# Kernel optimization log

Measured on AMD Instinct MI355X. Metric: run time of the kernel, lower is better.

The kernel has to match this reference:

```python
import jax, jax.numpy as jnp
import numpy as np

B, T, D, H, L, E, NL = 512, 360, 12, 256, 64, 8, 2


def _lstm_layer(x, h0, c0, Wih, Whh, bih, bhh):
    # x: [B, T, in_dim]; PyTorch gate order i, f, g, o
    b = bih + bhh
    def step(carry, xt):
        h, c = carry
        gates = xt @ Wih.T + h @ Whh.T + b  # [B, 4H]
        i, f, g, o = jnp.split(gates, 4, axis=-1)
        c = jax.nn.sigmoid(f) * c + jax.nn.sigmoid(i) * jnp.tanh(g)
        h = jax.nn.sigmoid(o) * jnp.tanh(c)
        return (h, c), h
    (hT, cT), ys = jax.lax.scan(step, (h0, c0), jnp.swapaxes(x, 0, 1))
    return jnp.swapaxes(ys, 0, 1), hT, cT


def _forward(x, eps, emb, Wih0f, Whh0f, bih0f, bhh0f, Wih0b, Whh0b, bih0b, bhh0b,
             Wih1f, Whh1f, bih1f, bhh1f, Wih1b, Whh1b, bih1b, bhh1b,
             Wmu, bmu, Wlv, blv, Whid, bhid, Wcell, bcell,
             dWih0, dWhh0, dbih0, dbhh0, dWih1, dWhh1, dbih1, dbhh1, Wout, bout, labels):
    Bn = x.shape[0]
    ce = emb[labels]  # [B, E]
    xc = jnp.concatenate([x, jnp.broadcast_to(ce[:, None, :], (Bn, T, E))], axis=-1)
    z0 = jnp.zeros((Bn, H), x.dtype)
    # encoder: 2-layer bidirectional LSTM
    yf0, _, _ = _lstm_layer(xc, z0, z0, Wih0f, Whh0f, bih0f, bhh0f)
    yb0, _, _ = _lstm_layer(xc[:, ::-1], z0, z0, Wih0b, Whh0b, bih0b, bhh0b)
    y0 = jnp.concatenate([yf0, yb0[:, ::-1]], axis=-1)  # [B, T, 2H]
    _, hf, _ = _lstm_layer(y0, z0, z0, Wih1f, Whh1f, bih1f, bhh1f)
    _, hb, _ = _lstm_layer(y0[:, ::-1], z0, z0, Wih1b, Whh1b, bih1b, bhh1b)
    hcat = jnp.concatenate([hf, hb], axis=-1)  # [B, 2H]
    mu = hcat @ Wmu.T + bmu
    logvar = hcat @ Wlv.T + blv
    z = mu + eps * jnp.exp(0.5 * logvar)
    zc = jnp.concatenate([z, ce], axis=-1)  # [B, L+E]
    # faithful to torch .view(num_layers, B, H) on a [B, NL*H] tensor (row-major reshape)
    hid = (zc @ Whid.T + bhid).reshape(NL, Bn, H)
    cel = (zc @ Wcell.T + bcell).reshape(NL, Bn, H)
    # decoder with full teacher forcing: step-t input is target step t-1 (zeros at t=0)
    shifted = jnp.concatenate([jnp.zeros((Bn, 1, D), x.dtype), x[:, :-1]], axis=1)
    din = jnp.concatenate([shifted, jnp.broadcast_to(zc[:, None, :], (Bn, T, L + E))], axis=-1)
    y0d, _, _ = _lstm_layer(din, hid[0], cel[0], dWih0, dWhh0, dbih0, dbhh0)
    y1d, _, _ = _lstm_layer(y0d, hid[1], cel[1], dWih1, dWhh1, dbih1, dbhh1)
    x_recon = y1d @ Wout.T + bout
    return x_recon, mu, logvar, z


def setup_inputs():
    key = jax.random.key(0)
    ki = iter(jax.random.split(key, 48))
    def rn(shape, s=0.05):
        return jax.random.normal(next(ki), shape, jnp.float32) * s
    inp = {}
    inp["x"] = jax.random.normal(next(ki), (B, T, D), jnp.float32)
    inp["labels"] = jax.random.randint(next(ki), (B,), 0, 2)
    inp["eps"] = jax.random.normal(next(ki), (B, L), jnp.float32)
    inp["emb"] = rn((2, E), 1.0)
    # encoder LSTM: layer0 input D+E, layer1 input 2H, forward/backward directions
    for name, idim in [("0f", D + E), ("0b", D + E), ("1f", 2 * H), ("1b", 2 * H)]:
        inp["Wih" + name] = rn((4 * H, idim))
        inp["Whh" + name] = rn((4 * H, H))
        inp["bih" + name] = rn((4 * H,))
        inp["bhh" + name] = rn((4 * H,))
    inp["Wmu"] = rn((L, 2 * H)); inp["bmu"] = rn((L,))
    inp["Wlv"] = rn((L, 2 * H)); inp["blv"] = rn((L,))
    inp["Whid"] = rn((NL * H, L + E)); inp["bhid"] = rn((NL * H,))
    inp["Wcell"] = rn((NL * H, L + E)); inp["bcell"] = rn((NL * H,))
    # decoder LSTM: layer0 input D + (L+E), layer1 input H
    inp["dWih0"] = rn((4 * H, D + L + E)); inp["dWhh0"] = rn((4 * H, H))
    inp["dbih0"] = rn((4 * H,)); inp["dbhh0"] = rn((4 * H,))
    inp["dWih1"] = rn((4 * H, H)); inp["dWhh1"] = rn((4 * H, H))
    inp["dbih1"] = rn((4 * H,)); inp["dbhh1"] = rn((4 * H,))
    inp["Wout"] = rn((D, H)); inp["bout"] = rn((D,))
    return inp


def reference(x, labels, eps, emb, Wih0f, Whh0f, bih0f, bhh0f, Wih0b, Whh0b, bih0b, bhh0b,
              Wih1f, Whh1f, bih1f, bhh1f, Wih1b, Whh1b, bih1b, bhh1b,
              Wmu, bmu, Wlv, blv, Whid, bhid, Wcell, bcell,
              dWih0, dWhh0, dbih0, dbhh0, dWih1, dWhh1, dbih1, dbhh1, Wout, bout):
    return _forward(x, eps, emb, Wih0f, Whh0f, bih0f, bhh0f, Wih0b, Whh0b, bih0b, bhh0b,
                    Wih1f, Whh1f, bih1f, bhh1f, Wih1b, Whh1b, bih1b, bhh1b,
                    Wmu, bmu, Wlv, blv, Whid, bhid, Wcell, bcell,
                    dWih0, dWhh0, dbih0, dbhh0, dWih1, dWhh1, dbih1, dbhh1, Wout, bout, labels)
```

## Files before the change

kernel.cpp:

```cpp
#include <hip/hip_runtime.h>
#include <cstdint>
#include <cstddef>

#define TT 360
#define BFULL 512
#define GH 1024

typedef unsigned short u16;
typedef short bf16x8_t __attribute__((ext_vector_type(8)));
typedef short bf16x4_t __attribute__((ext_vector_type(4)));
typedef float f32x4_t  __attribute__((ext_vector_type(4)));

#define MFMA(A,B,C) __builtin_amdgcn_mfma_f32_16x16x32_bf16(A,B,C,0,0,0)

__device__ __forceinline__ float bf2f(u16 u){
  union { unsigned u; float f; } v; v.u = ((unsigned)u) << 16; return v.f;
}
__device__ __forceinline__ u16 f2bf(float f){
  union { float f; unsigned u; } v; v.f = f;
  unsigned r = v.u + 0x7FFFu + ((v.u >> 16) & 1u);
  return (u16)(r >> 16);
}
__device__ __forceinline__ float sigm(float x){
  float e = __builtin_amdgcn_exp2f(-1.44269504089f * x);
  return __builtin_amdgcn_rcpf(1.f + e);
}
__device__ __forceinline__ float tanh_(float x){
  float e = __builtin_amdgcn_exp2f(-2.88539008178f * x);
  return 2.f * __builtin_amdgcn_rcpf(1.f + e) - 1.f;
}
__device__ __forceinline__ f32x4_t cvt4(bf16x4_t v){
  f32x4_t r;
#pragma unroll
  for (int i = 0; i < 4; ++i) r[i] = bf2f((u16)v[i]);
  return r;
}

__device__ __forceinline__ void st_u16_sc(void* p, u16 v){
  asm volatile("global_store_short %0, %1, off sc0 sc1" :: "v"(p), "v"(v) : "memory");
}
__device__ __forceinline__ void st_flag(int* p, int v){
  asm volatile("global_store_dword %0, %1, off sc0 sc1" :: "v"(p), "v"(v) : "memory");
}
__device__ __forceinline__ int ld_flag(const int* p){
  int v;
  asm volatile("global_load_dword %0, %1, off sc0 sc1\n\ts_waitcnt vmcnt(0)"
               : "=v"(v) : "v"(p) : "memory");
  return v;
}
__device__ __forceinline__ void ld2_b128_sc(const void* p0, const void* p1, f32x4_t* a, f32x4_t* b){
  asm volatile("global_load_dwordx4 %0, %2, off sc0 sc1\n\t"
               "global_load_dwordx4 %1, %3, off sc0 sc1\n\t"
               "s_waitcnt vmcnt(0)"
               : "=&v"(*a), "=&v"(*b) : "v"(p0), "v"(p1) : "memory");
}


__global__ void k_cvt_pad(const float* src, u16* dst, int N, int srcK, int useK, int Np, int Kp){
  int i = blockIdx.x * blockDim.x + threadIdx.x;
  if (i >= Np * Kp) return;
  int n = i / Kp, k = i - n * Kp;
  float v = (n < N && k < useK) ? src[(size_t)n * srcK + k] : 0.f;
  dst[i] = f2bf(v);
}

__global__ void k_repack(const float* src, u16* dst){
  int d = blockIdx.x * blockDim.x + threadIdx.x;
  if (d >= 262144) return;
  int e  = d & 7;
  int ln = (d >> 3) & 63;
  int ks = (d >> 9) & 7;
  int ct = (d >> 12) & 3;
  int g  = (d >> 14) & 3;
  int ns = (d >> 16) & 3;
  int c = ns * 64 + ct * 16 + (ln & 15);
  int n = g * 256 + c;
  int k = ks * 32 + (ln >> 4) * 8 + e;
  dst[d] = f2bf(src[n * 256 + k]);
}

__global__ void k_bias_sum(const float* a, const float* b, float* o, int n){
  int i = blockIdx.x * blockDim.x + threadIdx.x;
  if (i < n) o[i] = a[i] + b[i];
}

__global__ void k_zero(int* p, int n){
  int i = blockIdx.x * blockDim.x + threadIdx.x;
  if (i < n) p[i] = 0;
}


struct ProjArgs {
  const u16* A; const u16* W;
  const float* colbias;
  u16* G;
  int Akp, K, t0, rev, Bg, bgLog;
};

template<int BK>
__global__ __launch_bounds__(256) void k_proj(ProjArgs p){
  constexpr int SLOTS = BK / 8;
  constexpr int SM = SLOTS - 1;
  constexpr int LOG = (BK == 64) ? 3 : 2;
  __shared__ __align__(16) u16 lA[128 * BK];
  __shared__ __align__(16) u16 lW[128 * BK];
  const int tid = threadIdx.x, lane = tid & 63, wid = tid >> 6;
  const int wm = wid >> 1, wn = wid & 1;
  const int mBase = blockIdx.x * 128;
  const int nBase = blockIdx.y * 128;
  const int t_rel = mBase >> p.bgLog;
  const int bBase = mBase & (p.Bg - 1);
  const int t_glob = p.t0 + t_rel;
  const int t_src = p.rev ? (TT - 1 - t_glob) : t_glob;

  f32x4_t acc[4][4];
#pragma unroll
  for (int m = 0; m < 4; ++m)
#pragma unroll
    for (int n = 0; n < 4; ++n) acc[m][n] = (f32x4_t){0.f, 0.f, 0.f, 0.f};

  for (int k0 = 0; k0 < p.K; k0 += BK){
#pragma unroll
    for (int i = 0; i < (128 * SLOTS) / 256; ++i){
      int idx = i * 256 + tid;
      int row = idx >> LOG, sl = idx & SM;
      bf16x8_t va = *(const bf16x8_t*)(p.A + (size_t)((bBase + row) * TT + t_src) * p.Akp + k0 + sl * 8);
      *(bf16x8_t*)&lA[((row << LOG) + (sl ^ (row & SM))) * 8] = va;
      bf16x8_t vw = *(const bf16x8_t*)(p.W + (size_t)(nBase + row) * p.K + k0 + sl * 8);
      *(bf16x8_t*)&lW[((row << LOG) + (sl ^ (row & SM))) * 8] = vw;
    }
    __syncthreads();
#pragma unroll
    for (int kk = 0; kk < BK; kk += 32){
      bf16x8_t af[4], wf[4];
#pragma unroll
      for (int m = 0; m < 4; ++m){
        int row = wm * 64 + m * 16 + (lane & 15);
        int sl = ((kk >> 3) + (lane >> 4)) ^ (row & SM);
        af[m] = *(const bf16x8_t*)&lA[((row << LOG) + sl) * 8];
      }
#pragma unroll
      for (int n = 0; n < 4; ++n){
        int row = wn * 64 + n * 16 + (lane & 15);
        int sl = ((kk >> 3) + (lane >> 4)) ^ (row & SM);
        wf[n] = *(const bf16x8_t*)&lW[((row << LOG) + sl) * 8];
      }
#pragma unroll
      for (int m = 0; m < 4; ++m)
#pragma unroll
        for (int n = 0; n < 4; ++n)
          acc[m][n] = MFMA(af[m], wf[n], acc[m][n]);
    }
    __syncthreads();
  }

  const int btiles = p.Bg >> 4;
#pragma unroll
  for (int m = 0; m < 4; ++m){
    int btile = (bBase + wm * 64 + m * 16) >> 4;
#pragma unroll
    for (int n = 0; n < 4; ++n){
      int coltile = nBase + wn * 64 + n * 16;
      int col = coltile + (lane & 15);
      int ntile = coltile >> 4;
      float cb = p.colbias ? p.colbias[col] : 0.f;
      bf16x4_t outv;
#pragma unroll
      for (int q = 0; q < 4; ++q)
        outv[q] = (short)f2bf(acc[m][n][q] + cb);
      *(bf16x4_t*)(p.G + ((((size_t)t_rel * btiles + btile) * 64 + ntile) * 64 + lane) * 4) = outv;
    }
  }
}


struct RecArgs {
  const u16* Wr0; const u16* Wr1;
  int* flg0; int* flg1;
  u16* hX0; u16* hX1;
  const u16* G0; const u16* G1; int btilesG;
  const float* x; const int* labels; const float* emb; int gb0;
  const float* cb0; const float* cb1;
  const u16* Wx0; const u16* Wx1;
  const u16* zcF;
  const u16* hI0; const u16* hI1;
  const float* cI0; const float* cI1;
  float* cS0; float* cS1;
  u16* hW0; u16* hW1;
  u16* Y; int ycols; int yoff0; int yoff1;
  const u16* Wo; const float* bo; float* outp;
  int t0, t1, nbt;
};

template<int MODE>
__global__ __launch_bounds__(512, 1) void k_rec(RecArgs a){
  constexpr bool XIN  = (MODE <= 1);
  constexpr bool DEC  = (MODE == 1);
  constexpr bool GIN  = (MODE >= 2);
  constexpr bool OUTP = (MODE == 3);

  __shared__ __align__(16) u16 Wlds[65536];
  __shared__ __align__(16) u16 hlds[8192];
  __shared__ __align__(16) u16 xT[1024];

  const int bx = blockIdx.x;
  const int ns = bx & 3;
  const int gid = bx >> 2;
  const int dir = gid / a.nbt;
  const int bt = gid - dir * a.nbt;
  const int bb = bt * 32;
  const int tid = threadIdx.x;
  const int lane = tid & 63, w = tid >> 6;
  const int l15 = lane & 15, lhi = lane >> 4;
  const int mt = w >> 2, ct = w & 3;
  const int colb = ns * 64 + ct * 16 + l15;

  const u16* Wsrc = (dir ? a.Wr1 : a.Wr0) + (size_t)ns * 65536;
  int* flg = (dir ? a.flg1 : a.flg0) + bt * 4;
  u16* hXg = (dir ? a.hX1 : a.hX0) + (size_t)bt * 16384;
  const int yoff = dir ? a.yoff1 : a.yoff0;

#pragma unroll
  for (int i = 0; i < 16; ++i){
    int idx = i * 512 + tid;
    *(f32x4_t*)((char*)Wlds + (size_t)idx * 16) = *(const f32x4_t*)((const char*)Wsrc + (size_t)idx * 16);
  }

  float cfr[4];
  {
    const float* cp = dir ? a.cI1 : a.cI0;
#pragma unroll
    for (int q = 0; q < 4; ++q)
      cfr[q] = cp ? cp[(size_t)(bb + mt * 16 + lhi * 4 + q) * 256 + colb] : 0.f;
  }

  float bias4[4];
  f32x4_t zcv[4];
  bf16x8_t wfx[4];
  if (XIN && !DEC){
    const float* cb = dir ? a.cb1 : a.cb0;
#pragma unroll
    for (int g = 0; g < 4; ++g) bias4[g] = cb[g * 256 + colb];
  }
  if (DEC){
#pragma unroll
    for (int g = 0; g < 4; ++g){
      int ntile = g * 16 + ns * 4 + ct;
      bf16x4_t zv = *(const bf16x4_t*)(a.zcF + ((((size_t)((bb >> 4) + mt)) * 64 + ntile) * 64 + lane) * 4);
      zcv[g] = cvt4(zv);
    }
  }
  if (XIN){
    const u16* Wx = dir ? a.Wx1 : a.Wx0;
#pragma unroll
    for (int g = 0; g < 4; ++g)
      wfx[g] = *(const bf16x8_t*)(Wx + (size_t)(g * 256 + colb) * 32 + lhi * 8);
  }
  bf16x8_t wo8[8];
  float bo = 0.f;
  if (OUTP && ns == 0 && w < 2){
#pragma unroll
    for (int ks = 0; ks < 8; ++ks)
      wo8[ks] = *(const bf16x8_t*)(a.Wo + (size_t)l15 * 256 + ks * 32 + lhi * 8);
    if (l15 < 12) bo = a.bo[l15];
  }

  if (XIN){
    int row = tid >> 4, c16 = tid & 15;
    int gr = a.gb0 + bb + row;
    u16 vA = 0, vB = 0;
    if (!DEC){
      int lb = a.labels[gr];
      if (c16 >= 12) vA = f2bf(a.emb[lb * 8 + (c16 - 12)]);
      if (c16 < 4)   vB = f2bf(a.emb[lb * 8 + 4 + c16]);
    }
    u16 x0 = 0;
    if (!DEC && c16 < 12){
      int t0src = dir ? (TT - 1) : 0;
      x0 = f2bf(a.x[((size_t)gr * TT + t0src) * 12 + c16]);
    }
    xT[row * 32 + c16] = (c16 < 12) ? x0 : vA;
    xT[row * 32 + 16 + c16] = vB;
  }

  unsigned dsA[8];
#pragma unroll
  for (int ks = 0; ks < 8; ++ks)
    dsA[ks] = (unsigned)((((mt * 16 + l15) << 5) + (((ks << 2) + lhi) ^ (l15 & 7))) * 16);
  unsigned wrO[4];
#pragma unroll
  for (int q = 0; q < 4; ++q){
    int row = mt * 16 + lhi * 4 + q;
    wrO[q] = (unsigned)((row << 9) + (((colb >> 3) ^ (row & 7)) << 4) + ((colb & 7) << 1));
  }
  const char* Gc = GIN ? (const char*)(dir ? a.G1 : a.G0) : nullptr;
  unsigned gOff[4];
  const unsigned gstep = (unsigned)a.btilesG * 32768u;
  bf16x4_t gvP[4];
  if (GIN){
#pragma unroll
    for (int g = 0; g < 4; ++g){
      int ntile = g * 16 + ns * 4 + ct;
      gOff[g] = (unsigned)((((bb >> 4) + mt) * 64 + ntile) * 512 + lane * 8);
    }
#pragma unroll
    for (int g = 0; g < 4; ++g)
      gvP[g] = *(const bf16x4_t*)(Gc + gOff[g]);
  }

  if (a.t0 == 0){
    const u16* hp = dir ? a.hI1 : a.hI0;
#pragma unroll
    for (int q = 0; q < 4; ++q){
      u16 hv = hp ? hp[(size_t)(bb + mt * 16 + lhi * 4 + q) * 256 + colb] : (u16)0;
      st_u16_sc((char*)hXg + wrO[q], hv);
    }
  }
  __syncthreads();
  if (tid == 0 && a.t0 == 0) st_flag(flg + ns, 1);

  auto spin_to = [&](int target){
    if (w == 0){
      while (true){
        int f = (lane < 4) ? ld_flag(flg + lane) : target;
        if (__all(f >= target)) break;
        __builtin_amdgcn_s_sleep(2);
      }
    }
    __syncthreads();
  };
  auto stage_h = [&](int par){
    const char* src = (const char*)hXg + par * 16384;
    int o0 = (w * 2) * 1024 + lane * 16;
    f32x4_t v0, v1;
    ld2_b128_sc(src + o0, src + o0 + 1024, &v0, &v1);
    *(f32x4_t*)((char*)hlds + o0) = v0;
    *(f32x4_t*)((char*)hlds + o0 + 1024) = v1;
  };

  spin_to(a.t0 + 1);
  stage_h(a.t0 & 1);
  __syncthreads();

  for (int t = a.t0; t < a.t1; ++t){
    if (OUTP && ns == 0 && w < 2 && t > 0){
      f32x4_t oa = (f32x4_t){0.f, 0.f, 0.f, 0.f};
#pragma unroll
      for (int ks = 0; ks < 8; ++ks){
        bf16x8_t af = *(const bf16x8_t*)((char*)hlds + w * 8192 + dsA[ks]);
        oa = MFMA(af, wo8[ks], oa);
      }
      if (l15 < 12){
#pragma unroll
        for (int q = 0; q < 4; ++q)
          a.outp[((size_t)(bb + w * 16 + lhi * 4 + q) * TT + (t - 1)) * 12 + l15] = oa[q] + bo;
      }
    }
    f32x4_t acc[4];
    if (GIN){
#pragma unroll
      for (int g = 0; g < 4; ++g) acc[g] = cvt4(gvP[g]);
    } else if (DEC){
#pragma unroll
      for (int g = 0; g < 4; ++g) acc[g] = zcv[g];
    } else {
#pragma unroll
      for (int g = 0; g < 4; ++g) acc[g] = (f32x4_t){bias4[g], bias4[g], bias4[g], bias4[g]};
    }
    if (XIN){
      bf16x8_t ax = *(const bf16x8_t*)((char*)xT + (mt * 16 + l15) * 64 + lhi * 16);
#pragma unroll
      for (int g = 0; g < 4; ++g) acc[g] = MFMA(ax, wfx[g], acc[g]);
    }
#pragma unroll
    for (int ks = 0; ks < 8; ++ks){
      bf16x8_t af = *(const bf16x8_t*)((char*)hlds + dsA[ks]);
#pragma unroll
      for (int g = 0; g < 4; ++g){
        bf16x8_t bf = *(const bf16x8_t*)((char*)Wlds + ((g * 4 + ct) * 8 + ks) * 1024 + lane * 16);
        acc[g] = MFMA(af, bf, acc[g]);
      }
    }
    const int par = (t + 1) & 1;
    u16 hbv[4];
#pragma unroll
    for (int q = 0; q < 4; ++q){
      float iv = sigm(acc[0][q]);
      float fv = sigm(acc[1][q]);
      float gv = tanh_(acc[2][q]);
      float ov = sigm(acc[3][q]);
      float c = fv * cfr[q] + iv * gv;
      cfr[q] = c;
      u16 hb = f2bf(ov * tanh_(c));
      hbv[q] = hb;
      st_u16_sc((char*)hXg + par * 16384 + wrO[q], hb);
    }
    __syncthreads();
    if (tid == 0) st_flag(flg + ns, t + 2);
    if (XIN){
      const int ty = (MODE == 0 && dir) ? (TT - 1 - t) : t;
#pragma unroll
      for (int q = 0; q < 4; ++q)
        a.Y[((size_t)(bb + mt * 16 + lhi * 4 + q) * TT + ty) * a.ycols + yoff + colb] = hbv[q];
    }
    if (GIN){
#pragma unroll
      for (int g = 0; g < 4; ++g) gOff[g] += gstep;
      if (t + 1 < a.t1){
#pragma unroll
        for (int g = 0; g < 4; ++g)
          gvP[g] = *(const bf16x4_t*)(Gc + gOff[g]);
      }
    }
    spin_to(t + 2);
    stage_h(par);
    if (XIN && (t + 1) < a.t1){
      if (tid < 128 && (tid & 3) < 3){
        int row = tid >> 2, xq = tid & 3;
        int tsrc = DEC ? t : (dir ? (TT - 2 - t) : (t + 1));
        f32x4_t xv = *(const f32x4_t*)(a.x + ((size_t)(a.gb0 + bb + row) * TT + tsrc) * 12 + xq * 4);
        bf16x4_t xb;
#pragma unroll
        for (int e = 0; e < 4; ++e) xb[e] = (short)f2bf(xv[e]);
        *(bf16x4_t*)((char*)xT + row * 64 + xq * 8) = xb;
      }
    }
    __syncthreads();
  }

  if (OUTP && ns == 0 && w < 2){
    f32x4_t oa = (f32x4_t){0.f, 0.f, 0.f, 0.f};
#pragma unroll
    for (int ks = 0; ks < 8; ++ks){
      bf16x8_t af = *(const bf16x8_t*)((char*)hlds + w * 8192 + dsA[ks]);
      oa = MFMA(af, wo8[ks], oa);
    }
    if (l15 < 12){
#pragma unroll
      for (int q = 0; q < 4; ++q)
        a.outp[((size_t)(bb + w * 16 + lhi * 4 + q) * TT + (a.t1 - 1)) * 12 + l15] = oa[q] + bo;
    }
  }
  {
    float* cs = dir ? a.cS1 : a.cS0;
    if (cs){
#pragma unroll
      for (int q = 0; q < 4; ++q)
        cs[(size_t)(bb + mt * 16 + lhi * 4 + q) * 256 + colb] = cfr[q];
    }
    u16* hw = dir ? a.hW1 : a.hW0;
    if (hw){
#pragma unroll
      for (int q = 0; q < 4; ++q){
        u16 hv = *(u16*)((char*)hlds + wrO[q]);
        hw[(size_t)(bb + mt * 16 + lhi * 4 + q) * 256 + colb] = hv;
      }
    }
  }
}


__global__ void k_mulv(const u16* sH0, const u16* sH1,
                       const float* Wmu, const float* bmu,
                       const float* Wlv, const float* blv, float* mulv){
  int i = blockIdx.x * blockDim.x + threadIdx.x;
  if (i >= BFULL * 128) return;
  int b = i >> 7, j = i & 127;
  const float* W = (j < 64) ? (Wmu + (size_t)j * 512) : (Wlv + (size_t)(j - 64) * 512);
  float s = (j < 64) ? bmu[j] : blv[j - 64];
  for (int k = 0; k < 256; ++k) s += bf2f(sH0[(size_t)b * 256 + k]) * W[k];
  for (int k = 0; k < 256; ++k) s += bf2f(sH1[(size_t)b * 256 + k]) * W[256 + k];
  mulv[i] = s;
}

__global__ void k_sample(const float* mulv, const float* eps, const int* labels, const float* emb,
                         float* out_mu, float* out_lv, float* out_z, float* zcf){
  int i = blockIdx.x * blockDim.x + threadIdx.x;
  if (i >= BFULL * 128) return;
  int b = i >> 7, j = i & 127;
  if (j < 64){
    float mu = mulv[b * 128 + j];
    float lv = mulv[b * 128 + 64 + j];
    float z = mu + eps[b * 64 + j] * __expf(0.5f * lv);
    out_mu[b * 64 + j] = mu;
    out_lv[b * 64 + j] = lv;
    out_z[b * 64 + j] = z;
    zcf[i] = z;
  } else if (j < 72){
    zcf[i] = emb[labels[b] * 8 + (j - 64)];
  } else {
    zcf[i] = 0.f;
  }
}

__global__ void k_hc(const float* zcf, const float* Whid, const float* bhid,
                     const float* Wcell, const float* bcell, float* HC){
  int i = blockIdx.x * blockDim.x + threadIdx.x;
  if (i >= BFULL * 1024) return;
  int b = i >> 10, n = i & 1023;
  const float* W; float s;
  if (n < 512){ W = Whid + (size_t)n * 72; s = bhid[n]; }
  else        { W = Wcell + (size_t)(n - 512) * 72; s = bcell[n - 512]; }
  for (int k = 0; k < 72; ++k) s += zcf[b * 128 + k] * W[k];
  HC[i] = s;
}

__global__ void k_zconst(const float* zcf, const float* dWih0,
                         const float* dbih0, const float* dbhh0, float* zconst){
  int i = blockIdx.x * blockDim.x + threadIdx.x;
  if (i >= BFULL * 1024) return;
  int b = i >> 10, n = i & 1023;
  float s = dbih0[n] + dbhh0[n];
  const float* W = dWih0 + (size_t)n * 84 + 12;
  for (int k = 0; k < 72; ++k) s += zcf[b * 128 + k] * W[k];
  zconst[i] = s;
}

__global__ void k_zfrag(const float* zconst, u16* zcF){
  int i = blockIdx.x * blockDim.x + threadIdx.x;
  if (i >= BFULL * GH) return;
  int q = i & 3, ln = (i >> 2) & 63, nt = (i >> 8) & 63, bt = i >> 14;
  int r = bt * 16 + (ln >> 4) * 4 + q;
  int col = nt * 16 + (ln & 15);
  zcF[i] = f2bf(zconst[(size_t)r * GH + col]);
}

__global__ void k_dec_init(const float* HC, u16* h0, float* c0, u16* h1, float* c1){
  int i = blockIdx.x * blockDim.x + threadIdx.x;
  if (i >= BFULL * 256) return;
  int b = i >> 8, h = i & 255;
  int col = (b & 1) * 256 + h;
  int r0 = b >> 1;
  int r1 = 256 + (b >> 1);
  h0[i] = f2bf(HC[(size_t)r0 * 1024 + col]);
  c0[i] =      HC[(size_t)r0 * 1024 + 512 + col];
  h1[i] = f2bf(HC[(size_t)r1 * 1024 + col]);
  c1[i] =      HC[(size_t)r1 * 1024 + 512 + col];
}


static inline size_t alignup(size_t x){ return (x + 255) & ~(size_t)255; }
static inline int ilog2(int x){ return 31 - __builtin_clz((unsigned)x); }

extern "C" void kernel_launch(void* const* d_in, const int* in_sizes, int n_in,
                              void* d_out, int out_size, void* d_ws, size_t ws_size,
                              hipStream_t stream){
  const float* x      = (const float*)d_in[0];
  const int*   labels = (const int*)  d_in[1];
  const float* eps    = (const float*)d_in[2];
  const float* emb    = (const float*)d_in[3];
  const float* Wih0f = (const float*)d_in[4],  *Whh0f = (const float*)d_in[5];
  const float* bih0f = (const float*)d_in[6],  *bhh0f = (const float*)d_in[7];
  const float* Wih0b = (const float*)d_in[8],  *Whh0b = (const float*)d_in[9];
  const float* bih0b = (const float*)d_in[10], *bhh0b = (const float*)d_in[11];
  const float* Wih1f = (const float*)d_in[12], *Whh1f = (const float*)d_in[13];
  const float* bih1f = (const float*)d_in[14], *bhh1f = (const float*)d_in[15];
  const float* Wih1b = (const float*)d_in[16], *Whh1b = (const float*)d_in[17];
  const float* bih1b = (const float*)d_in[18], *bhh1b = (const float*)d_in[19];
  const float* Wmu = (const float*)d_in[20], *bmu = (const float*)d_in[21];
  const float* Wlv = (const float*)d_in[22], *blv = (const float*)d_in[23];
  const float* Whid = (const float*)d_in[24], *bhid = (const float*)d_in[25];
  const float* Wcell = (const float*)d_in[26], *bcell = (const float*)d_in[27];
  const float* dWih0 = (const float*)d_in[28], *dWhh0 = (const float*)d_in[29];
  const float* dbih0 = (const float*)d_in[30], *dbhh0 = (const float*)d_in[31];
  const float* dWih1 = (const float*)d_in[32], *dWhh1 = (const float*)d_in[33];
  const float* dbih1 = (const float*)d_in[34], *dbhh1 = (const float*)d_in[35];
  const float* Wout = (const float*)d_in[36], *bout = (const float*)d_in[37];

  float* out = (float*)d_out;
  float* out_mu = out + (size_t)BFULL * TT * 12;
  float* out_lv = out_mu + (size_t)BFULL * 64;
  float* out_z  = out_lv + (size_t)BFULL * 64;

  char* ws = (char*)d_ws; size_t off = 0;
  auto alloc = [&](size_t bytes)->char*{ char* p = ws + off; off += alignup(bytes); return p; };

  u16* W0f_b  = (u16*)alloc(1024 * 32 * 2);
  u16* W0b_b  = (u16*)alloc(1024 * 32 * 2);
  u16* dWx_b  = (u16*)alloc(1024 * 32 * 2);
  u16* Wo_b   = (u16*)alloc(16 * 256 * 2);
  u16* Whh0f_r = (u16*)alloc((size_t)1024 * 256 * 2);
  u16* Whh0b_r = (u16*)alloc((size_t)1024 * 256 * 2);
  u16* Whh1f_r = (u16*)alloc((size_t)1024 * 256 * 2);
  u16* Whh1b_r = (u16*)alloc((size_t)1024 * 256 * 2);
  u16* dWhh0_r = (u16*)alloc((size_t)1024 * 256 * 2);
  u16* dWhh1_r = (u16*)alloc((size_t)1024 * 256 * 2);
  u16* dWih1_b = (u16*)alloc((size_t)1024 * 256 * 2);
  u16* Wih1f_b = (u16*)alloc((size_t)1024 * 512 * 2);
  u16* Wih1b_b = (u16*)alloc((size_t)1024 * 512 * 2);
  float* b0f = (float*)alloc(1024 * 4);
  float* b0b = (float*)alloc(1024 * 4);
  float* b1f = (float*)alloc(1024 * 4);
  float* b1b = (float*)alloc(1024 * 4);
  float* db1 = (float*)alloc(1024 * 4);
  u16*  sHe1 = (u16*)alloc((size_t)2 * BFULL * 256 * 2);
  float* sCe1 = (float*)alloc((size_t)2 * BFULL * 256 * 4);
  u16*  dh0 = (u16*)alloc((size_t)BFULL * 256 * 2);
  float* dc0 = (float*)alloc((size_t)BFULL * 256 * 4);
  u16*  dh1 = (u16*)alloc((size_t)BFULL * 256 * 2);
  float* dc1 = (float*)alloc((size_t)BFULL * 256 * 4);
  float* mulv = (float*)alloc((size_t)BFULL * 128 * 4);
  float* zcf  = (float*)alloc((size_t)BFULL * 128 * 4);
  float* HC   = (float*)alloc((size_t)BFULL * 1024 * 4);
  float* zconst = (float*)alloc((size_t)BFULL * 1024 * 4);
  u16*  zcF   = (u16*)alloc((size_t)BFULL * 1024 * 2);
  int*  flagsA = (int*)alloc(512 * 4);
  u16*  hXA    = (u16*)alloc((size_t)2 * 16 * 16384 * 2);

  size_t rem = (ws_size > off + (1 << 20)) ? ws_size - off - (1 << 20) : 0;
  int eb = 128, Tc = 2;
  {
    const int sch[][2] = {
      {512,360},{512,120},{512,40},{512,24},{512,12},{512,8},
      {256,360},{256,120},{256,40},{256,12},{256,8},
      {128,360},{128,40},{128,8},{128,2}};
    for (int i = 0; i < (int)(sizeof(sch)/sizeof(sch[0])); ++i){
      size_t need = alignup((size_t)sch[i][0] * TT * 512 * 2)
                  + 2 * alignup((size_t)sch[i][1] * sch[i][0] * GH * 2);
      if (need <= rem){ eb = sch[i][0]; Tc = sch[i][1]; break; }
    }
  }
  const int ebLog = ilog2(eb);
  const int nGroups = BFULL / eb;
  const int nbt = eb / 32;

  u16* y0 = (u16*)alloc((size_t)eb * TT * 512 * 2);
  u16* Gf = (u16*)alloc((size_t)Tc * eb * GH * 2);
  u16* Gb = (u16*)alloc((size_t)Tc * eb * GH * 2);
  u16* y0d = y0;

  auto cvt = [&](const float* src, u16* dst, int N, int srcK, int useK, int Np, int Kp){
    int tot = Np * Kp;
    k_cvt_pad<<<(tot + 255) / 256, 256, 0, stream>>>(src, dst, N, srcK, useK, Np, Kp);
  };
  auto repack = [&](const float* src, u16* dst){
    k_repack<<<1024, 256, 0, stream>>>(src, dst);
  };
  auto bsum = [&](const float* a, const float* b, float* o){
    k_bias_sum<<<4, 256, 0, stream>>>(a, b, o, 1024);
  };
  auto proj = [&](const u16* A, int Akp, int K, const u16* W, const float* cbp,
                  u16* G, int t0, int tc, int rev){
    ProjArgs pa; pa.A = A; pa.W = W; pa.colbias = cbp; pa.G = G;
    pa.Akp = Akp; pa.K = K; pa.t0 = t0; pa.rev = rev; pa.Bg = eb; pa.bgLog = ebLog;
    dim3 grid(tc * (eb / 128), 8);
    k_proj<64><<<grid, 256, 0, stream>>>(pa);
  };
  auto flgbase = [&](int layer, int d, int gb0){ return flagsA + ((layer * 2 + d) * 16 + (gb0 >> 5)) * 4; };
  auto hxbase  = [&](int d, int gb0){ return hXA + ((size_t)d * 16 + (gb0 >> 5)) * 16384; };

  k_zero<<<2, 256, 0, stream>>>(flagsA, 512);
  cvt(Wih0f, W0f_b, 1024, 20, 20, 1024, 32);
  cvt(Wih0b, W0b_b, 1024, 20, 20, 1024, 32);
  cvt(dWih0, dWx_b, 1024, 84, 12, 1024, 32);
  cvt(Wout,  Wo_b,  12, 256, 256, 16, 256);
  repack(Whh0f, Whh0f_r);
  repack(Whh0b, Whh0b_r);
  repack(Whh1f, Whh1f_r);
  repack(Whh1b, Whh1b_r);
  repack(dWhh0, dWhh0_r);
  repack(dWhh1, dWhh1_r);
  cvt(dWih1, dWih1_b, 1024, 256, 256, 1024, 256);
  cvt(Wih1f, Wih1f_b, 1024, 512, 512, 1024, 512);
  cvt(Wih1b, Wih1b_b, 1024, 512, 512, 1024, 512);
  bsum(bih0f, bhh0f, b0f);
  bsum(bih0b, bhh0b, b0b);
  bsum(bih1f, bhh1f, b1f);
  bsum(bih1b, bhh1b, b1b);
  bsum(dbih1, dbhh1, db1);

  for (int g = 0; g < nGroups; ++g){
    int gb0 = g * eb;
    {
      RecArgs ra = {};
      ra.Wr0 = Whh0f_r; ra.Wr1 = Whh0b_r;
      ra.flg0 = flgbase(0, 0, gb0); ra.flg1 = flgbase(0, 1, gb0);
      ra.hX0 = hxbase(0, gb0); ra.hX1 = hxbase(1, gb0);
      ra.x = x; ra.labels = labels; ra.emb = emb; ra.gb0 = gb0;
      ra.cb0 = b0f; ra.cb1 = b0b;
      ra.Wx0 = W0f_b; ra.Wx1 = W0b_b;
      ra.Y = y0; ra.ycols = 512; ra.yoff0 = 0; ra.yoff1 = 256;
      ra.t0 = 0; ra.t1 = TT; ra.nbt = nbt;
      k_rec<0><<<2 * nbt * 4, 512, 0, stream>>>(ra);
    }
    for (int t0 = 0; t0 < TT; t0 += Tc){
      int t1 = (t0 + Tc < TT) ? t0 + Tc : TT; int tc = t1 - t0;
      proj(y0, 512, 512, Wih1f_b, b1f, Gf, t0, tc, 0);
      proj(y0, 512, 512, Wih1b_b, b1b, Gb, t0, tc, 1);
      RecArgs ra = {};
      ra.Wr0 = Whh1f_r; ra.Wr1 = Whh1b_r;
      ra.flg0 = flgbase(1, 0, gb0); ra.flg1 = flgbase(1, 1, gb0);
      ra.hX0 = hxbase(0, gb0); ra.hX1 = hxbase(1, gb0);
      ra.G0 = Gf; ra.G1 = Gb; ra.btilesG = eb >> 4;
      ra.cI0 = t0 ? (sCe1 + (size_t)gb0 * 256) : nullptr;
      ra.cI1 = t0 ? (sCe1 + (size_t)BFULL * 256 + (size_t)gb0 * 256) : nullptr;
      ra.cS0 = sCe1 + (size_t)gb0 * 256;
      ra.cS1 = sCe1 + (size_t)BFULL * 256 + (size_t)gb0 * 256;
      ra.hW0 = sHe1 + (size_t)gb0 * 256;
      ra.hW1 = sHe1 + (size_t)BFULL * 256 + (size_t)gb0 * 256;
      ra.t0 = t0; ra.t1 = t1; ra.nbt = nbt;
      k_rec<2><<<2 * nbt * 4, 512, 0, stream>>>(ra);
    }
  }

  k_mulv<<<(BFULL * 128) / 256, 256, 0, stream>>>(sHe1, sHe1 + (size_t)BFULL * 256,
                                                  Wmu, bmu, Wlv, blv, mulv);
  k_sample<<<(BFULL * 128) / 256, 256, 0, stream>>>(mulv, eps, labels, emb,
                                                    out_mu, out_lv, out_z, zcf);
  k_hc<<<(BFULL * 1024) / 256, 256, 0, stream>>>(zcf, Whid, bhid, Wcell, bcell, HC);
  k_zconst<<<(BFULL * 1024) / 256, 256, 0, stream>>>(zcf, dWih0, dbih0, dbhh0, zconst);
  k_zfrag<<<(BFULL * GH) / 256, 256, 0, stream>>>(zconst, zcF);
  k_dec_init<<<(BFULL * 256) / 256, 256, 0, stream>>>(HC, dh0, dc0, dh1, dc1);

  for (int g = 0; g < nGroups; ++g){
    int gb0 = g * eb;
    {
      RecArgs ra = {};
      ra.Wr0 = dWhh0_r; ra.Wr1 = dWhh0_r;
      ra.flg0 = flgbase(2, 0, gb0); ra.flg1 = flgbase(2, 0, gb0);
      ra.hX0 = hxbase(0, gb0); ra.hX1 = hxbase(0, gb0);
      ra.x = x; ra.gb0 = gb0;
      ra.zcF = zcF + ((size_t)(gb0 >> 4)) * 16384;
      ra.Wx0 = dWx_b; ra.Wx1 = dWx_b;
      ra.hI0 = dh0 + (size_t)gb0 * 256;
      ra.cI0 = dc0 + (size_t)gb0 * 256;
      ra.Y = y0d; ra.ycols = 256; ra.yoff0 = 0; ra.yoff1 = 0;
      ra.t0 = 0; ra.t1 = TT; ra.nbt = nbt;
      k_rec<1><<<nbt * 4, 512, 0, stream>>>(ra);
    }
    for (int t0 = 0; t0 < TT; t0 += Tc){
      int t1 = (t0 + Tc < TT) ? t0 + Tc : TT; int tc = t1 - t0;
      proj(y0d, 256, 256, dWih1_b, db1, Gf, t0, tc, 0);
      RecArgs ra = {};
      ra.Wr0 = dWhh1_r; ra.Wr1 = dWhh1_r;
      ra.flg0 = flgbase(3, 0, gb0); ra.flg1 = flgbase(3, 0, gb0);
      ra.hX0 = hxbase(0, gb0); ra.hX1 = hxbase(0, gb0);
      ra.G0 = Gf; ra.G1 = Gf; ra.btilesG = eb >> 4;
      ra.hI0 = dh1 + (size_t)gb0 * 256;
      ra.cI0 = t0 ? (sCe1 + (size_t)gb0 * 256) : (dc1 + (size_t)gb0 * 256);
      ra.cS0 = sCe1 + (size_t)gb0 * 256;
      ra.Wo = Wo_b; ra.bo = bout;
      ra.outp = out + (size_t)gb0 * TT * 12;
      ra.t0 = t0; ra.t1 = t1; ra.nbt = nbt;
      k_rec<3><<<nbt * 4, 512, 0, stream>>>(ra);
    }
  }
}
```

Baseline: 5.783 ms.

## Fuse decoder layer-1 recurrence into layer-0 kernel as wavefront-pipelined blocks

Decoder layer 0 and layer 1 now run concurrently in a single persistent launch. Extra blocks compute layer 1 one step behind layer 0, synchronised through global flags. Layer 1's input and recurrent weights are concatenated into one K=512 LDS-resident matrix, so the separate chunked input-projection GEMM and its G buffer are dropped. The output head now lives in the layer-1 blocks. The cost is 1.5x more co-resident blocks, extra cross-layer flag spinning, and higher per-block MFMA work for layer 1, with a deadlock risk if not all blocks are co-resident.

Result: faster. 4.934 ms, median of 2 (-14.7%).

```diff
diff --git a/kernel.cpp b/kernel.cpp
--- a/kernel.cpp
+++ b/kernel.cpp
@@ -53,6 +53,16 @@
                "global_load_dwordx4 %1, %3, off sc0 sc1\n\t"
                "s_waitcnt vmcnt(0)"
                : "=&v"(*a), "=&v"(*b) : "v"(p0), "v"(p1) : "memory");
+}
+__device__ __forceinline__ void ld4_b128_sc(const void* p0, const void* p1, const void* p2, const void* p3,
+                                            f32x4_t* a, f32x4_t* b, f32x4_t* c, f32x4_t* d){
+  asm volatile("global_load_dwordx4 %0, %4, off sc0 sc1\n\t"
+               "global_load_dwordx4 %1, %5, off sc0 sc1\n\t"
+               "global_load_dwordx4 %2, %6, off sc0 sc1\n\t"
+               "global_load_dwordx4 %3, %7, off sc0 sc1\n\t"
+               "s_waitcnt vmcnt(0)"
+               : "=&v"(*a), "=&v"(*b), "=&v"(*c), "=&v"(*d)
+               : "v"(p0), "v"(p1), "v"(p2), "v"(p3) : "memory");
 }
 
 
@@ -77,6 +87,21 @@
   int n = g * 256 + c;
   int k = ks * 32 + (ln >> 4) * 8 + e;
   dst[d] = f2bf(src[n * 256 + k]);
+}
+
+__global__ void k_repack_cat(const float* Wih, const float* Whh, u16* dst){
+  int d = blockIdx.x * blockDim.x + threadIdx.x;
+  if (d >= 524288) return;
+  int e   = d & 7;
+  int ln  = (d >> 3) & 63;
+  int ks  = (d >> 9) & 15;
+  int ct  = (d >> 13) & 1;
+  int g   = (d >> 14) & 3;
+  int ns8 = (d >> 16) & 7;
+  int n = g * 256 + ns8 * 32 + ct * 16 + (ln & 15);
+  int k = ks * 32 + (ln >> 4) * 8 + e;
+  float v = (k < 256) ? Wih[(size_t)n * 256 + k] : Whh[(size_t)n * 256 + (k - 256)];
+  dst[d] = f2bf(v);
 }
 
 __global__ void k_bias_sum(const float* a, const float* b, float* o, int n){
@@ -194,36 +219,190 @@
 
 template<int MODE>
 __global__ __launch_bounds__(512, 1) void k_rec(RecArgs a){
+  constexpr bool ENC0 = (MODE == 0);
+  constexpr bool DEC  = (MODE == 1);
+  constexpr bool GIN  = (MODE == 2);
   constexpr bool XIN  = (MODE <= 1);
-  constexpr bool DEC  = (MODE == 1);
-  constexpr bool GIN  = (MODE >= 2);
-  constexpr bool OUTP = (MODE == 3);
-
-  __shared__ __align__(16) u16 Wlds[65536];
-  __shared__ __align__(16) u16 hlds[8192];
-  __shared__ __align__(16) u16 xT[1024];
+
+  __shared__ __align__(16) char S[163840];
+  u16* Wlds = (u16*)S;
+  u16* hlds = (u16*)(S + 131072);
+  u16* hl1  = (u16*)(S + 147456);
+  u16* xT   = (u16*)(S + 147456);
 
   const int bx = blockIdx.x;
-  const int ns = bx & 3;
-  const int gid = bx >> 2;
-  const int dir = gid / a.nbt;
-  const int bt = gid - dir * a.nbt;
-  const int bb = bt * 32;
   const int tid = threadIdx.x;
   const int lane = tid & 63, w = tid >> 6;
   const int l15 = lane & 15, lhi = lane >> 4;
+
+  if (DEC && bx >= a.nbt * 4){
+    const int idx = bx - a.nbt * 4;
+    const int ns8 = idx & 7;
+    const int bt = idx >> 3;
+    const int bb = bt * 32;
+    const int mt = (w >> 1) & 1, ct = w & 1;
+    const int colb = ns8 * 32 + ct * 16 + l15;
+    const u16* Wsrc = a.Wr1 + (size_t)ns8 * 65536;
+    int* ownflg = a.flg1 + bt * 8;
+    const int* l0flg = a.flg0 + bt * 4;
+    u16* hXo = a.hX1 + (size_t)bt * 16384;
+    const u16* hXl0 = a.hX0 + (size_t)bt * 16384;
+
+#pragma unroll
+    for (int i = 0; i < 16; ++i){
+      int ix = i * 512 + tid;
+      *(f32x4_t*)((char*)Wlds + (size_t)ix * 16) = *(const f32x4_t*)((const char*)Wsrc + (size_t)ix * 16);
+    }
+    float cfr[4], bias4[4];
+    if (w < 4){
+#pragma unroll
+      for (int g = 0; g < 4; ++g) bias4[g] = a.cb1[g * 256 + colb];
+#pragma unroll
+      for (int q = 0; q < 4; ++q)
+        cfr[q] = a.cI1[(size_t)(bb + mt * 16 + lhi * 4 + q) * 256 + colb];
+    }
+    bf16x8_t wo8[8];
+    float bo = 0.f;
+    if (ns8 == 0 && (w == 4 || w == 5)){
+#pragma unroll
+      for (int ks = 0; ks < 8; ++ks)
+        wo8[ks] = *(const bf16x8_t*)(a.Wo + (size_t)l15 * 256 + ks * 32 + lhi * 8);
+      if (l15 < 12) bo = a.bo[l15];
+    }
+    unsigned dsA[8];
+#pragma unroll
+    for (int ks = 0; ks < 8; ++ks)
+      dsA[ks] = (unsigned)((((mt * 16 + l15) << 5) + (((ks << 2) + lhi) ^ (l15 & 7))) * 16);
+    unsigned wrO[4];
+    if (w < 4){
+#pragma unroll
+      for (int q = 0; q < 4; ++q){
+        int row = mt * 16 + lhi * 4 + q;
+        wrO[q] = (unsigned)((row << 9) + (((colb >> 3) ^ (row & 7)) << 4) + ((colb & 7) << 1));
+      }
+#pragma unroll
+      for (int q = 0; q < 4; ++q){
+        u16 hv = a.hI1[(size_t)(bb + mt * 16 + lhi * 4 + q) * 256 + colb];
+        st_u16_sc((char*)hXo + wrO[q], hv);
+      }
+    }
+    __syncthreads();
+    if (tid == 0) st_flag(ownflg + ns8, 1);
+
+    auto spinL1 = [&](int tOwn, int tL0, int useL0){
+      if (w == 0){
+        while (true){
+          int f = 0x7fffffff, tgt = 0;
+          if (lane < 8){ f = ld_flag(ownflg + lane); tgt = tOwn; }
+          else if (lane < 12 && useL0){ f = ld_flag((const int*)l0flg + (lane - 8)); tgt = tL0; }
+          if (__all(f >= tgt)) break;
+          __builtin_amdgcn_s_sleep(2);
+        }
+      }
+      __syncthreads();
+    };
+    auto stage2 = [&](int parA, int parB, int doA){
+      int o0 = w * 2048 + lane * 16;
+      const char* sB = (const char*)hXo + parB * 16384;
+      f32x4_t v0, v1, v2, v3;
+      if (doA){
+        const char* sA = (const char*)hXl0 + parA * 16384;
+        ld4_b128_sc(sA + o0, sA + o0 + 1024, sB + o0, sB + o0 + 1024, &v0, &v1, &v2, &v3);
+        *(f32x4_t*)((char*)hlds + o0) = v0;
+        *(f32x4_t*)((char*)hlds + o0 + 1024) = v1;
+      } else {
+        ld2_b128_sc(sB + o0, sB + o0 + 1024, &v2, &v3);
+      }
+      *(f32x4_t*)((char*)hl1 + o0) = v2;
+      *(f32x4_t*)((char*)hl1 + o0 + 1024) = v3;
+    };
+
+    spinL1(1, 2, 1);
+    stage2(1, 0, 1);
+    __syncthreads();
+
+    for (int t = 0; t < TT; ++t){
+      if (ns8 == 0 && (w == 4 || w == 5) && t > 0){
+        f32x4_t oa = (f32x4_t){0.f, 0.f, 0.f, 0.f};
+#pragma unroll
+        for (int ks = 0; ks < 8; ++ks){
+          bf16x8_t af = *(const bf16x8_t*)((char*)hl1 + (w - 4) * 8192 + dsA[ks]);
+          oa = MFMA(af, wo8[ks], oa);
+        }
+        if (l15 < 12){
+#pragma unroll
+          for (int q = 0; q < 4; ++q)
+            a.outp[((size_t)(bb + (w - 4) * 16 + lhi * 4 + q) * TT + (t - 1)) * 12 + l15] = oa[q] + bo;
+        }
+      }
+      const int par = (t + 1) & 1;
+      if (w < 4){
+        f32x4_t acc[4];
+#pragma unroll
+        for (int g = 0; g < 4; ++g) acc[g] = (f32x4_t){bias4[g], bias4[g], bias4[g], bias4[g]};
+#pragma unroll
+        for (int ks = 0; ks < 16; ++ks){
+          bf16x8_t af = (ks < 8)
+            ? *(const bf16x8_t*)((char*)hlds + dsA[ks])
+            : *(const bf16x8_t*)((char*)hl1 + dsA[ks - 8]);
+#pragma unroll
+          for (int g = 0; g < 4; ++g){
+            bf16x8_t bf = *(const bf16x8_t*)((char*)Wlds + ((g * 2 + ct) * 16 + ks) * 1024 + lane * 16);
+            acc[g] = MFMA(af, bf, acc[g]);
+          }
+        }
+#pragma unroll
+        for (int q = 0; q < 4; ++q){
+          float iv = sigm(acc[0][q]);
+          float fv = sigm(acc[1][q]);
+          float gv = tanh_(acc[2][q]);
+          float ov = sigm(acc[3][q]);
+          float c = fv * cfr[q] + iv * gv;
+          cfr[q] = c;
+          st_u16_sc((char*)hXo + par * 16384 + wrO[q], f2bf(ov * tanh_(c)));
+        }
+      }
+      __syncthreads();
+      if (tid == 0) st_flag(ownflg + ns8, t + 2);
+      int more = (t + 1 < TT);
+      spinL1(t + 2, t + 3, more);
+      stage2(t & 1, par, more);
+      __syncthreads();
+    }
+    if (ns8 == 0 && (w == 4 || w == 5)){
+      f32x4_t oa = (f32x4_t){0.f, 0.f, 0.f, 0.f};
+#pragma unroll
+      for (int ks = 0; ks < 8; ++ks){
+        bf16x8_t af = *(const bf16x8_t*)((char*)hl1 + (w - 4) * 8192 + dsA[ks]);
+        oa = MFMA(af, wo8[ks], oa);
+      }
+      if (l15 < 12){
+#pragma unroll
+        for (int q = 0; q < 4; ++q)
+          a.outp[((size_t)(bb + (w - 4) * 16 + lhi * 4 + q) * TT + (TT - 1)) * 12 + l15] = oa[q] + bo;
+      }
+    }
+    return;
+  }
+
+  const int ns = bx & 3;
+  const int gid = bx >> 2;
+  const int dir = DEC ? 0 : (gid / a.nbt);
+  const int bt = DEC ? gid : (gid - dir * a.nbt);
+  const int bb = bt * 32;
   const int mt = w >> 2, ct = w & 3;
   const int colb = ns * 64 + ct * 16 + l15;
 
   const u16* Wsrc = (dir ? a.Wr1 : a.Wr0) + (size_t)ns * 65536;
   int* flg = (dir ? a.flg1 : a.flg0) + bt * 4;
+  const int* l1flg = DEC ? (a.flg1 + bt * 8) : nullptr;
   u16* hXg = (dir ? a.hX1 : a.hX0) + (size_t)bt * 16384;
   const int yoff = dir ? a.yoff1 : a.yoff0;
 
 #pragma unroll
   for (int i = 0; i < 16; ++i){
-    int idx = i * 512 + tid;
-    *(f32x4_t*)((char*)Wlds + (size_t)idx * 16) = *(const f32x4_t*)((const char*)Wsrc + (size_t)idx * 16);
+    int ix = i * 512 + tid;
+    *(f32x4_t*)((char*)Wlds + (size_t)ix * 16) = *(const f32x4_t*)((const char*)Wsrc + (size_t)ix * 16);
   }
 
   float cfr[4];
@@ -237,7 +416,7 @@
   float bias4[4];
   f32x4_t zcv[4];
   bf16x8_t wfx[4];
-  if (XIN && !DEC){
+  if (ENC0){
     const float* cb = dir ? a.cb1 : a.cb0;
 #pragma unroll
     for (int g = 0; g < 4; ++g) bias4[g] = cb[g * 256 + colb];
@@ -255,14 +434,6 @@
 #pragma unroll
     for (int g = 0; g < 4; ++g)
       wfx[g] = *(const bf16x8_t*)(Wx + (size_t)(g * 256 + colb) * 32 + lhi * 8);
-  }
-  bf16x8_t wo8[8];
-  float bo = 0.f;
-  if (OUTP && ns == 0 && w < 2){
-#pragma unroll
-    for (int ks = 0; ks < 8; ++ks)
-      wo8[ks] = *(const bf16x8_t*)(a.Wo + (size_t)l15 * 256 + ks * 32 + lhi * 8);
-    if (l15 < 12) bo = a.bo[l15];
   }
 
   if (XIN){
@@ -310,20 +481,23 @@
 
   if (a.t0 == 0){
     const u16* hp = dir ? a.hI1 : a.hI0;
+    const u16* hq = DEC ? a.hI0 : hp;
 #pragma unroll
     for (int q = 0; q < 4; ++q){
-      u16 hv = hp ? hp[(size_t)(bb + mt * 16 + lhi * 4 + q) * 256 + colb] : (u16)0;
+      u16 hv = hq ? hq[(size_t)(bb + mt * 16 + lhi * 4 + q) * 256 + colb] : (u16)0;
       st_u16_sc((char*)hXg + wrO[q], hv);
     }
   }
   __syncthreads();
   if (tid == 0 && a.t0 == 0) st_flag(flg + ns, 1);
 
-  auto spin_to = [&](int target){
+  auto spin_to = [&](int tOwn, int tL1){
     if (w == 0){
       while (true){
-        int f = (lane < 4) ? ld_flag(flg + lane) : target;
-        if (__all(f >= target)) break;
+        int f = 0x7fffffff, tgt = 0;
+        if (lane < 4){ f = ld_flag(flg + lane); tgt = tOwn; }
+        else if (DEC && lane < 12){ f = ld_flag((const int*)l1flg + (lane - 4)); tgt = tL1; }
+        if (__all(f >= tgt)) break;
         __builtin_amdgcn_s_sleep(2);
       }
     }
@@ -331,31 +505,18 @@
   };
   auto stage_h = [&](int par){
     const char* src = (const char*)hXg + par * 16384;
-    int o0 = (w * 2) * 1024 + lane * 16;
+    int o0 = w * 2048 + lane * 16;
     f32x4_t v0, v1;
     ld2_b128_sc(src + o0, src + o0 + 1024, &v0, &v1);
     *(f32x4_t*)((char*)hlds + o0) = v0;
     *(f32x4_t*)((char*)hlds + o0 + 1024) = v1;
   };
 
-  spin_to(a.t0 + 1);
+  spin_to(a.t0 + 1, 0);
   stage_h(a.t0 & 1);
   __syncthreads();
 
   for (int t = a.t0; t < a.t1; ++t){
-    if (OUTP && ns == 0 && w < 2 && t > 0){
-      f32x4_t oa = (f32x4_t){0.f, 0.f, 0.f, 0.f};
-#pragma unroll
-      for (int ks = 0; ks < 8; ++ks){
-        bf16x8_t af = *(const bf16x8_t*)((char*)hlds + w * 8192 + dsA[ks]);
-        oa = MFMA(af, wo8[ks], oa);
-      }
-      if (l15 < 12){
-#pragma unroll
-        for (int q = 0; q < 4; ++q)
-          a.outp[((size_t)(bb + w * 16 + lhi * 4 + q) * TT + (t - 1)) * 12 + l15] = oa[q] + bo;
-      }
-    }
     f32x4_t acc[4];
     if (GIN){
 #pragma unroll
@@ -397,8 +558,8 @@
     }
     __syncthreads();
     if (tid == 0) st_flag(flg + ns, t + 2);
-    if (XIN){
-      const int ty = (MODE == 0 && dir) ? (TT - 1 - t) : t;
+    if (ENC0){
+      const int ty = dir ? (TT - 1 - t) : t;
 #pragma unroll
       for (int q = 0; q < 4; ++q)
         a.Y[((size_t)(bb + mt * 16 + lhi * 4 + q) * TT + ty) * a.ycols + yoff + colb] = hbv[q];
@@ -412,7 +573,7 @@
           gvP[g] = *(const bf16x4_t*)(Gc + gOff[g]);
       }
     }
-    spin_to(t + 2);
+    spin_to(t + 2, t + 1);
     stage_h(par);
     if (XIN && (t + 1) < a.t1){
       if (tid < 128 && (tid & 3) < 3){
@@ -428,19 +589,6 @@
     __syncthreads();
   }
 
-  if (OUTP && ns == 0 && w < 2){
-    f32x4_t oa = (f32x4_t){0.f, 0.f, 0.f, 0.f};
-#pragma unroll
-    for (int ks = 0; ks < 8; ++ks){
-      bf16x8_t af = *(const bf16x8_t*)((char*)hlds + w * 8192 + dsA[ks]);
-      oa = MFMA(af, wo8[ks], oa);
-    }
-    if (l15 < 12){
-#pragma unroll
-      for (int q = 0; q < 4; ++q)
-        a.outp[((size_t)(bb + w * 16 + lhi * 4 + q) * TT + (a.t1 - 1)) * 12 + l15] = oa[q] + bo;
-    }
-  }
   {
     float* cs = dir ? a.cS1 : a.cS0;
     if (cs){
@@ -584,8 +732,7 @@
   u16* Whh1f_r = (u16*)alloc((size_t)1024 * 256 * 2);
   u16* Whh1b_r = (u16*)alloc((size_t)1024 * 256 * 2);
   u16* dWhh0_r = (u16*)alloc((size_t)1024 * 256 * 2);
-  u16* dWhh1_r = (u16*)alloc((size_t)1024 * 256 * 2);
-  u16* dWih1_b = (u16*)alloc((size_t)1024 * 256 * 2);
+  u16* Wcat_r  = (u16*)alloc((size_t)1024 * 512 * 2);
   u16* Wih1f_b = (u16*)alloc((size_t)1024 * 512 * 2);
   u16* Wih1b_b = (u16*)alloc((size_t)1024 * 512 * 2);
   float* b0f = (float*)alloc(1024 * 4);
@@ -604,7 +751,8 @@
   float* HC   = (float*)alloc((size_t)BFULL * 1024 * 4);
   float* zconst = (float*)alloc((size_t)BFULL * 1024 * 4);
   u16*  zcF   = (u16*)alloc((size_t)BFULL * 1024 * 2);
-  int*  flagsA = (int*)alloc(512 * 4);
+  int*  flagsA = (int*)alloc(768 * 4);
+  int*  flagsB = flagsA + 512;
   u16*  hXA    = (u16*)alloc((size_t)2 * 16 * 16384 * 2);
 
   size_t rem = (ws_size > off + (1 << 20)) ? ws_size - off - (1 << 20) : 0;
@@ -627,7 +775,6 @@
   u16* y0 = (u16*)alloc((size_t)eb * TT * 512 * 2);
   u16* Gf = (u16*)alloc((size_t)Tc * eb * GH * 2);
   u16* Gb = (u16*)alloc((size_t)Tc * eb * GH * 2);
-  u16* y0d = y0;
 
   auto cvt = [&](const float* src, u16* dst, int N, int srcK, int useK, int Np, int Kp){
     int tot = Np * Kp;
@@ -649,7 +796,7 @@
   auto flgbase = [&](int layer, int d, int gb0){ return flagsA + ((layer * 2 + d) * 16 + (gb0 >> 5)) * 4; };
   auto hxbase  = [&](int d, int gb0){ return hXA + ((size_t)d * 16 + (gb0 >> 5)) * 16384; };
 
-  k_zero<<<2, 256, 0, stream>>>(flagsA, 512);
+  k_zero<<<3, 256, 0, stream>>>(flagsA, 768);
   cvt(Wih0f, W0f_b, 1024, 20, 20, 1024, 32);
   cvt(Wih0b, W0b_b, 1024, 20, 20, 1024, 32);
   cvt(dWih0, dWx_b, 1024, 84, 12, 1024, 32);
@@ -659,8 +806,7 @@
   repack(Whh1f, Whh1f_r);
   repack(Whh1b, Whh1b_r);
   repack(dWhh0, dWhh0_r);
-  repack(dWhh1, dWhh1_r);
-  cvt(dWih1, dWih1_b, 1024, 256, 256, 1024, 256);
+  k_repack_cat<<<2048, 256, 0, stream>>>(dWih1, dWhh1, Wcat_r);
   cvt(Wih1f, Wih1f_b, 1024, 512, 512, 1024, 512);
   cvt(Wih1b, Wih1b_b, 1024, 512, 512, 1024, 512);
   bsum(bih0f, bhh0f, b0f);
@@ -714,35 +860,21 @@
 
   for (int g = 0; g < nGroups; ++g){
     int gb0 = g * eb;
-    {
-      RecArgs ra = {};
-      ra.Wr0 = dWhh0_r; ra.Wr1 = dWhh0_r;
-      ra.flg0 = flgbase(2, 0, gb0); ra.flg1 = flgbase(2, 0, gb0);
-      ra.hX0 = hxbase(0, gb0); ra.hX1 = hxbase(0, gb0);
-      ra.x = x; ra.gb0 = gb0;
-      ra.zcF = zcF + ((size_t)(gb0 >> 4)) * 16384;
-      ra.Wx0 = dWx_b; ra.Wx1 = dWx_b;
-      ra.hI0 = dh0 + (size_t)gb0 * 256;
-      ra.cI0 = dc0 + (size_t)gb0 * 256;
-      ra.Y = y0d; ra.ycols = 256; ra.yoff0 = 0; ra.yoff1 = 0;
-      ra.t0 = 0; ra.t1 = TT; ra.nbt = nbt;
-      k_rec<1><<<nbt * 4, 512, 0, stream>>>(ra);
-    }
-    for (int t0 = 0; t0 < TT; t0 += Tc){
-      int t1 = (t0 + Tc < TT) ? t0 + Tc : TT; int tc = t1 - t0;
-      proj(y0d, 256, 256, dWih1_b, db1, Gf, t0, tc, 0);
-      RecArgs ra = {};
-      ra.Wr0 = dWhh1_r; ra.Wr1 = dWhh1_r;
-      ra.flg0 = flgbase(3, 0, gb0); ra.flg1 = flgbase(3, 0, gb0);
-      ra.hX0 = hxbase(0, gb0); ra.hX1 = hxbase(0, gb0);
-      ra.G0 = Gf; ra.G1 = Gf; ra.btilesG = eb >> 4;
-      ra.hI0 = dh1 + (size_t)gb0 * 256;
-      ra.cI0 = t0 ? (sCe1 + (size_t)gb0 * 256) : (dc1 + (size_t)gb0 * 256);
-      ra.cS0 = sCe1 + (size_t)gb0 * 256;
-      ra.Wo = Wo_b; ra.bo = bout;
-      ra.outp = out + (size_t)gb0 * TT * 12;
-      ra.t0 = t0; ra.t1 = t1; ra.nbt = nbt;
-      k_rec<3><<<nbt * 4, 512, 0, stream>>>(ra);
-    }
-  }
-}
+    RecArgs ra = {};
+    ra.Wr0 = dWhh0_r; ra.Wr1 = Wcat_r;
+    ra.flg0 = flgbase(2, 0, gb0); ra.flg1 = flagsB + (gb0 >> 5) * 8;
+    ra.hX0 = hxbase(0, gb0); ra.hX1 = hxbase(1, gb0);
+    ra.x = x; ra.gb0 = gb0;
+    ra.zcF = zcF + ((size_t)(gb0 >> 4)) * 16384;
+    ra.Wx0 = dWx_b; ra.Wx1 = dWx_b;
+    ra.hI0 = dh0 + (size_t)gb0 * 256;
+    ra.cI0 = dc0 + (size_t)gb0 * 256;
+    ra.hI1 = dh1 + (size_t)gb0 * 256;
+    ra.cI1 = dc1 + (size_t)gb0 * 256;
+    ra.cb1 = db1;
+    ra.Wo = Wo_b; ra.bo = bout;
+    ra.outp = out + (size_t)gb0 * TT * 12;
+    ra.t0 = 0; ra.t1 = TT; ra.nbt = nbt;
+    k_rec<1><<<nbt * 12, 512, 0, stream>>>(ra);
+  }
+}
```
